# Optimization experiments

Hardware: AMD Instinct MI355X
Metric: run time of the kernel (lower is better)

The kernel has to match this reference:

```python
import jax, jax.numpy as jnp
import numpy as np

N_NODES = 131072       # 64 graphs * 2048 nodes
N_EDGES = 2097152      # avg degree 16
N_GRAPHS = 64
NODES_PER_GRAPH = 2048
D_IN = 128
D_EMB = 64
D_HID = 128
N_ACT = 2048


def setup_inputs() -> dict:
    key = jax.random.key(0)
    ks = jax.random.split(key, 12)
    s = lambda d: 1.0 / np.sqrt(d)
    return {
        "x": jax.random.normal(ks[0], (N_NODES, D_IN), dtype=jnp.float32),
        "edge_index": jax.random.randint(ks[1], (2, N_EDGES), 0, N_NODES, dtype=jnp.int32),
        "W1l": jax.random.normal(ks[2], (D_EMB, D_IN), dtype=jnp.float32) * s(D_IN),
        "b1l": jnp.zeros((D_EMB,), dtype=jnp.float32),
        "W1r": jax.random.normal(ks[3], (D_EMB, D_IN), dtype=jnp.float32) * s(D_IN),
        "W2l": jax.random.normal(ks[4], (D_EMB, D_EMB), dtype=jnp.float32) * s(D_EMB),
        "b2l": jnp.zeros((D_EMB,), dtype=jnp.float32),
        "W2r": jax.random.normal(ks[5], (D_EMB, D_EMB), dtype=jnp.float32) * s(D_EMB),
        "fc1_W": jax.random.normal(ks[6], (D_HID, D_EMB), dtype=jnp.float32) * s(D_EMB),
        "fc1_b": jnp.zeros((D_HID,), dtype=jnp.float32),
        "fc2_W": jax.random.normal(ks[7], (N_ACT, D_HID), dtype=jnp.float32) * s(D_HID),
        "fc2_b": jnp.zeros((N_ACT,), dtype=jnp.float32),
    }


def _sage_conv(x, src, dst, Wl, bl, Wr):
    # PyG SAGEConv (mean aggr): out = lin_l(mean_{j in N(i)} x_j) + lin_r(x_i)
    msg = x[src]                                              # [E, D] gather
    agg = jax.ops.segment_sum(msg, dst, num_segments=N_NODES)  # [N, D]
    cnt = jax.ops.segment_sum(jnp.ones((src.shape[0],), x.dtype), dst,
                              num_segments=N_NODES)
    mean = agg / jnp.maximum(cnt, 1.0)[:, None]
    return mean @ Wl.T + bl + x @ Wr.T


def reference(x, edge_index, W1l, b1l, W1r, W2l, b2l, W2r,
              fc1_W, fc1_b, fc2_W, fc2_b):
    src, dst = edge_index[0], edge_index[1]
    h1 = _sage_conv(x, src, dst, W1l, b1l, W1r)    # [N, D_EMB]
    h2 = _sage_conv(h1, src, dst, W2l, b2l, W2r)   # [N, D_EMB]
    g = h2.reshape(N_GRAPHS, NODES_PER_GRAPH, D_EMB).mean(axis=1)  # [B, D_EMB]
    h = jax.nn.relu(g @ fc1_W.T + fc1_b)
    q_values = h @ fc2_W.T + fc2_b                 # [B, N_ACT]
    return q_values
```

## Files before the change

### kernel.cpp

```cpp
#include <hip/hip_runtime.h>
#include <hip/hip_bf16.h>

#define D_IN 128
#define D_EMB 64

typedef float f32x2 __attribute__((ext_vector_type(2)));
typedef float f32x4v __attribute__((ext_vector_type(4)));
typedef short bf16x8 __attribute__((ext_vector_type(8)));

static __device__ __forceinline__ unsigned short f2bf(float f) {
  __hip_bfloat16 h = __float2bfloat16(f);
  return *(unsigned short*)&h;
}

__global__ __launch_bounds__(256) void wprep_mfma_k(const float* __restrict__ W,
                                                    unsigned short* __restrict__ out,
                                                    int K) {
  int tid = blockIdx.x * 256 + threadIdx.x;
  int total = (K / 32) * 4 * 64;
  if (tid >= total) return;
  int lane = tid & 63;
  int ct = (tid >> 6) & 3;
  int s = tid >> 8;
  int row = ct * 16 + (lane & 15);
  int kk = s * 32 + (lane >> 4) * 8;
  unsigned short tmp[8];
#pragma unroll
  for (int j = 0; j < 8; j++) tmp[j] = f2bf(W[row * K + kk + j]);
  *(uint4*)&out[(size_t)tid * 8] = *(uint4*)tmp;
}


__global__ __launch_bounds__(256) void bhist1_k(const int* __restrict__ dst,
                                                int* __restrict__ bh, int E) {
  __shared__ int h[256];
  const int t = threadIdx.x;
  h[t] = 0;
  __syncthreads();
  const int base = blockIdx.x * 2048;
#pragma unroll
  for (int j = 0; j < 8; j++) {
    int e = base + j * 256 + t;
    if (e < E) atomicAdd(&h[dst[e] >> 9], 1);
  }
  __syncthreads();
  bh[t * 1024 + blockIdx.x] = h[t];
}

__global__ __launch_bounds__(256) void scanA_k(int* __restrict__ bh,
                                               int* __restrict__ bintot) {
  __shared__ int sa[256], sb[256];
  const int t = threadIdx.x;
  int* row = bh + (size_t)blockIdx.x * 1024;
  int v0 = row[t * 4], v1 = row[t * 4 + 1], v2 = row[t * 4 + 2], v3 = row[t * 4 + 3];
  int sum = v0 + v1 + v2 + v3;
  sa[t] = sum;
  __syncthreads();
  int* in = sa;
  int* out = sb;
  for (int st = 1; st < 256; st <<= 1) {
    out[t] = in[t] + (t >= st ? in[t - st] : 0);
    __syncthreads();
    int* tmp = in; in = out; out = tmp;
  }
  int excl = in[t] - sum;
  row[t * 4] = excl;
  row[t * 4 + 1] = excl + v0;
  row[t * 4 + 2] = excl + v0 + v1;
  row[t * 4 + 3] = excl + v0 + v1 + v2;
  if (t == 255) bintot[blockIdx.x] = in[255];
}

__global__ __launch_bounds__(256) void scanB_k(const int* __restrict__ bintot,
                                               int* __restrict__ sbase) {
  __shared__ int sa[256], sb[256];
  const int t = threadIdx.x;
  int v = bintot[t];
  sa[t] = v;
  __syncthreads();
  int* in = sa;
  int* out = sb;
  for (int st = 1; st < 256; st <<= 1) {
    out[t] = in[t] + (t >= st ? in[t - st] : 0);
    __syncthreads();
    int* tmp = in; in = out; out = tmp;
  }
  sbase[t] = in[t] - v;
  if (t == 255) sbase[256] = in[255];
}

__global__ __launch_bounds__(256) void bfill1_k(const int* __restrict__ src,
                                                const int* __restrict__ dst,
                                                const int* __restrict__ bh,
                                                const int* __restrict__ sbase,
                                                unsigned int* __restrict__ bkt,
                                                int E) {
  __shared__ int hA[256], hB[256], runCur[256], gb[256];
  __shared__ int dcache[2048];
  __shared__ unsigned int sorted[2048];
  __shared__ unsigned short subb[2048];
  const int t = threadIdx.x;
  const int base = blockIdx.x * 2048;
  const int n = min(2048, E - base);
  hA[t] = 0;
  __syncthreads();
#pragma unroll
  for (int j = 0; j < 8; j++) {
    int idx = j * 256 + t;
    int e = base + idx;
    if (idx < n) {
      int d = dst[e];
      dcache[idx] = d;
      atomicAdd(&hA[d >> 9], 1);
    }
  }
  __syncthreads();
  int cnt = hA[t];
  int* in = hA;
  int* out = hB;
  for (int st = 1; st < 256; st <<= 1) {
    out[t] = in[t] + (t >= st ? in[t - st] : 0);
    __syncthreads();
    int* tmp = in; in = out; out = tmp;
  }
  int rs = in[t] - cnt;
  __syncthreads();
  hB[t] = rs;
  runCur[t] = rs;
  gb[t] = sbase[t] + bh[t * 1024 + blockIdx.x];
  __syncthreads();
#pragma unroll
  for (int j = 0; j < 8; j++) {
    int idx = j * 256 + t;
    int e = base + idx;
    if (idx < n) {
      int d = dcache[idx];
      int b = d >> 9;
      int lpos = atomicAdd(&runCur[b], 1);
      sorted[lpos] = ((unsigned)(d & 511) << 17) | (unsigned)src[e];
      subb[lpos] = (unsigned short)b;
    }
  }
  __syncthreads();
  for (int idx = t; idx < n; idx += 256) {
    int b = subb[idx];
    bkt[gb[b] + idx - hB[b]] = sorted[idx];
  }
}

__global__ __launch_bounds__(256) void deg4_k(const unsigned int* __restrict__ bkt,
                                              const int* __restrict__ sbase,
                                              int* __restrict__ deg) {
  __shared__ int h[512];
  const int t = threadIdx.x;
  h[t] = 0;
  h[t + 256] = 0;
  __syncthreads();
  const int i = blockIdx.x;
  const int lo = sbase[i], hi = sbase[i + 1];
  for (int e = lo + t; e < hi; e += 256) atomicAdd(&h[bkt[e] >> 17], 1);
  __syncthreads();
  deg[i * 512 + t] = h[t];
  deg[i * 512 + t + 256] = h[t + 256];
}

__global__ __launch_bounds__(256) void blocksum_k(const int* __restrict__ deg,
                                                  int* __restrict__ bsum) {
  __shared__ int sm[256];
  int t = threadIdx.x;
  sm[t] = deg[blockIdx.x * 256 + t];
  __syncthreads();
  for (int s = 128; s > 0; s >>= 1) {
    if (t < s) sm[t] += sm[t + s];
    __syncthreads();
  }
  if (t == 0) bsum[blockIdx.x] = sm[0];
}

__global__ __launch_bounds__(256) void scanbsum_k(int* __restrict__ bsum) {
  __shared__ int a[512], b[512];
  int t = threadIdx.x;
  a[t] = bsum[t];
  a[t + 256] = bsum[t + 256];
  __syncthreads();
  int* in = a;
  int* out = b;
  for (int st = 1; st < 512; st <<= 1) {
    for (int i = t; i < 512; i += 256) out[i] = in[i] + (i >= st ? in[i - st] : 0);
    __syncthreads();
    int* tmp = in; in = out; out = tmp;
  }
  for (int i = t; i < 512; i += 256) bsum[i] = (i == 0) ? 0 : in[i - 1];
}

__global__ __launch_bounds__(256) void rowptr_k(const int* __restrict__ deg,
                                                const int* __restrict__ bsumEx,
                                                int* __restrict__ rowPtr,
                                                float* __restrict__ invdeg) {
  __shared__ int a[256], b[256];
  int t = threadIdx.x;
  int i = blockIdx.x * 256 + t;
  int d = deg[i];
  a[t] = d;
  __syncthreads();
  int* in = a;
  int* out = b;
  for (int st = 1; st < 256; st <<= 1) {
    out[t] = in[t] + (t >= st ? in[t - st] : 0);
    __syncthreads();
    int* tmp = in; in = out; out = tmp;
  }
  int incl = in[t] + bsumEx[blockIdx.x];
  rowPtr[i + 1] = incl;
  invdeg[i] = 1.0f / fmaxf((float)d, 1.0f);
  if (i == 0) rowPtr[0] = 0;
}

#define CSR_CAP 12032
__global__ __launch_bounds__(256) void scat4_k(const unsigned int* __restrict__ bkt,
                                               const int* __restrict__ sbase,
                                               const int* __restrict__ rowPtr,
                                               int* __restrict__ csr) {
  __shared__ int cur[512];
  __shared__ int cbuf[CSR_CAP];
  const int t = threadIdx.x;
  const int i = blockIdx.x;
  const int node0 = i * 512;
  const int base0 = rowPtr[node0];
  cur[t] = rowPtr[node0 + t] - base0;
  cur[t + 256] = rowPtr[node0 + t + 256] - base0;
  __syncthreads();
  const int lo = sbase[i], hi = sbase[i + 1];
  for (int e = lo + t; e < hi; e += 256) {
    unsigned v = bkt[e];
    int pos = atomicAdd(&cur[v >> 17], 1);
    int sval = (int)(v & 0x1FFFFu);
    if (pos < CSR_CAP) cbuf[pos] = sval;
    else csr[base0 + pos] = sval;
  }
  __syncthreads();
  const int cnt = rowPtr[node0 + 512] - base0;
  const int lim = cnt < CSR_CAP ? cnt : CSR_CAP;
  for (int idx = t; idx < lim; idx += 256) csr[base0 + idx] = cbuf[idx];
}

template <int K, int DUAL>
__global__ __launch_bounds__(256) void gemm_mfma_k(const float4* __restrict__ x4,
                                                   const unsigned short* __restrict__ wb1,
                                                   const unsigned short* __restrict__ wb2,
                                                   const float* __restrict__ bias2,
                                                   unsigned char* __restrict__ out1,
                                                   float* __restrict__ out2) {
  constexpr int K4 = K / 4;
  constexpr int LROW = K + 8;
  __shared__ unsigned short sxb[64 * LROW];
  const int t = threadIdx.x;
  const int nb = blockIdx.x * 64;
#pragma unroll
  for (int idx = t; idx < 64 * K4; idx += 256) {
    int node = idx / K4, k4 = idx - node * K4;
    float4 v = x4[(size_t)(nb + node) * K4 + k4];
    ushort4 h;
    h.x = f2bf(v.x); h.y = f2bf(v.y); h.z = f2bf(v.z); h.w = f2bf(v.w);
    *(ushort4*)&sxb[node * LROW + k4 * 4] = h;
  }
  __syncthreads();
  const int lane = t & 63;
  const int wv = t >> 6;
  const int col = lane & 15;
  const int quad = lane >> 4;
  f32x4v acc1[4], acc2[4];
#pragma unroll
  for (int ct = 0; ct < 4; ct++) {
    acc1[ct] = (f32x4v){0.f, 0.f, 0.f, 0.f};
    if (DUAL) {
      float bj = bias2[ct * 16 + col];
      acc2[ct] = (f32x4v){bj, bj, bj, bj};
    }
  }
#pragma unroll
  for (int s = 0; s < K / 32; s++) {
    bf16x8 a = *(const bf16x8*)&sxb[(wv * 16 + col) * LROW + s * 32 + quad * 8];
#pragma unroll
    for (int ct = 0; ct < 4; ct++) {
      bf16x8 b1 = *(const bf16x8*)&wb1[(size_t)((s * 4 + ct) * 64 + lane) * 8];
      acc1[ct] = __builtin_amdgcn_mfma_f32_16x16x32_bf16(a, b1, acc1[ct], 0, 0, 0);
      if (DUAL) {
        bf16x8 b2 = *(const bf16x8*)&wb2[(size_t)((s * 4 + ct) * 64 + lane) * 8];
        acc2[ct] = __builtin_amdgcn_mfma_f32_16x16x32_bf16(a, b2, acc2[ct], 0, 0, 0);
      }
    }
  }
#pragma unroll
  for (int ct = 0; ct < 4; ct++) {
#pragma unroll
    for (int reg = 0; reg < 4; reg++) {
      int node = nb + wv * 16 + quad * 4 + reg;
      unsigned pk = (unsigned)__builtin_amdgcn_cvt_pk_fp8_f32(acc1[ct][reg],
                                                              acc1[ct][reg], 0, false);
      out1[(size_t)node * 64 + ct * 16 + col] = (unsigned char)(pk & 0xff);
      if (DUAL) out2[(size_t)node * 64 + ct * 16 + col] = acc2[ct][reg];
    }
  }
}

template <int WRITE_H>
__global__ __launch_bounds__(256) void gather_k(const uint4* __restrict__ yb,
                                                const int* __restrict__ csr,
                                                const int* __restrict__ rowPtr,
                                                const float* __restrict__ invdeg,
                                                float4* __restrict__ hio,
                                                float* __restrict__ pm) {
  __shared__ float sg[4][4][16];
  const int t = threadIdx.x;
  const int lane = t & 63;
  const int wv = t >> 6;
  const int q = lane & 3;
  const int nl = lane >> 2;
  const int nb = blockIdx.x * 64;
  const int n = nb + wv * 16 + nl;
  const int rp0 = rowPtr[n], rp1 = rowPtr[n + 1];
  float acc[16];
#pragma unroll
  for (int k = 0; k < 16; k++) acc[k] = 0.f;
  for (int e = rp0; e < rp1; e++) {
    int s = csr[e];
    uint4 v = yb[(size_t)s * 4 + q];
    f32x2 p;
    p = __builtin_amdgcn_cvt_pk_f32_fp8(v.x, false); acc[0] += p.x;  acc[1] += p.y;
    p = __builtin_amdgcn_cvt_pk_f32_fp8(v.x, true);  acc[2] += p.x;  acc[3] += p.y;
    p = __builtin_amdgcn_cvt_pk_f32_fp8(v.y, false); acc[4] += p.x;  acc[5] += p.y;
    p = __builtin_amdgcn_cvt_pk_f32_fp8(v.y, true);  acc[6] += p.x;  acc[7] += p.y;
    p = __builtin_amdgcn_cvt_pk_f32_fp8(v.z, false); acc[8] += p.x;  acc[9] += p.y;
    p = __builtin_amdgcn_cvt_pk_f32_fp8(v.z, true);  acc[10] += p.x; acc[11] += p.y;
    p = __builtin_amdgcn_cvt_pk_f32_fp8(v.w, false); acc[12] += p.x; acc[13] += p.y;
    p = __builtin_amdgcn_cvt_pk_f32_fp8(v.w, true);  acc[14] += p.x; acc[15] += p.y;
  }
  const float sc = invdeg[n];
  float gacc[16];
  if (WRITE_H) {
#pragma unroll
    for (int u = 0; u < 4; u++) {
      float4 o = hio[(size_t)n * 16 + q * 4 + u];
      float4 h = make_float4(acc[4 * u + 0] * sc + o.x, acc[4 * u + 1] * sc + o.y,
                             acc[4 * u + 2] * sc + o.z, acc[4 * u + 3] * sc + o.w);
      hio[(size_t)n * 16 + q * 4 + u] = h;
      gacc[4 * u + 0] = h.x; gacc[4 * u + 1] = h.y;
      gacc[4 * u + 2] = h.z; gacc[4 * u + 3] = h.w;
    }
  } else {
#pragma unroll
    for (int k = 0; k < 16; k++) gacc[k] = acc[k] * sc;
  }
#pragma unroll
  for (int m = 4; m <= 32; m <<= 1)
#pragma unroll
    for (int k = 0; k < 16; k++) gacc[k] += __shfl_xor(gacc[k], m, 64);
  if (nl == 0) {
#pragma unroll
    for (int k = 0; k < 16; k++) sg[wv][q][k] = gacc[k];
  }
  __syncthreads();
  if (t < 64) {
    int qq = t >> 4, k = t & 15;
    float tot = sg[0][qq][k] + sg[1][qq][k] + sg[2][qq][k] + sg[3][qq][k];
    pm[((size_t)(blockIdx.x >> 5) * 32 + (blockIdx.x & 31)) * 64 + t] = tot;
  }
}

__global__ __launch_bounds__(256) void reduce_part_k(const float* __restrict__ pm,
                                                     float* __restrict__ gm) {
  int idx = blockIdx.x * 256 + threadIdx.x;
  int b = idx >> 6, j = idx & 63;
  float acc = 0.0f;
  for (int blk = 0; blk < 32; blk++) acc += pm[((size_t)b * 32 + blk) * 64 + j];
  gm[idx] = acc * (1.0f / 2048.0f);
}

__global__ __launch_bounds__(256) void combine_k(const float* __restrict__ gmean2,
                                                 const float* __restrict__ gmean1,
                                                 const float* __restrict__ b2l,
                                                 const float* __restrict__ W2r,
                                                 float* __restrict__ g) {
  int idx = blockIdx.x * 256 + threadIdx.x;
  int b = idx >> 6, j = idx & 63;
  const float4* m4 = (const float4*)(gmean1 + b * 64);
  const float4* w4 = (const float4*)(W2r + j * 64);
  float acc = gmean2[idx] + b2l[j];
#pragma unroll
  for (int k4 = 0; k4 < 16; k4++) {
    float4 mv = m4[k4], wv = w4[k4];
    acc += mv.x * wv.x + mv.y * wv.y + mv.z * wv.z + mv.w * wv.w;
  }
  g[idx] = acc;
}

__global__ __launch_bounds__(256) void mlp1_k(const float* __restrict__ g,
                                              const float* __restrict__ fc1_W,
                                              const float* __restrict__ fc1_b,
                                              float* __restrict__ h) {
  int idx = blockIdx.x * 256 + threadIdx.x;
  int b = idx >> 7, k = idx & 127;
  const float4* g4 = (const float4*)(g + b * 64);
  const float4* w4 = (const float4*)(fc1_W + k * 64);
  float acc = fc1_b[k];
#pragma unroll
  for (int j4 = 0; j4 < 16; j4++) {
    float4 gv = g4[j4], wv = w4[j4];
    acc += gv.x * wv.x + gv.y * wv.y + gv.z * wv.z + gv.w * wv.w;
  }
  h[idx] = fmaxf(acc, 0.0f);
}

__global__ __launch_bounds__(256) void mlp2_k(const float* __restrict__ h,
                                              const float* __restrict__ fc2_W,
                                              const float* __restrict__ fc2_b,
                                              float* __restrict__ out) {
  __shared__ float4 sh[32];
  int b = blockIdx.x >> 3;
  int a = (blockIdx.x & 7) * 256 + threadIdx.x;
  if (threadIdx.x < 32) sh[threadIdx.x] = ((const float4*)(h + b * 128))[threadIdx.x];
  __syncthreads();
  const float4* w4 = (const float4*)(fc2_W + (size_t)a * 128);
  float acc = fc2_b[a];
#pragma unroll
  for (int k4 = 0; k4 < 32; k4++) {
    float4 hv = sh[k4], wv = w4[k4];
    acc += hv.x * wv.x + hv.y * wv.y + hv.z * wv.z + hv.w * wv.w;
  }
  out[b * 2048 + a] = acc;
}

extern "C" void kernel_launch(void* const* d_in, const int* in_sizes, int n_in,
                              void* d_out, int out_size, void* d_ws, size_t ws_size,
                              hipStream_t stream) {
  const float* x     = (const float*)d_in[0];
  const int*   ei    = (const int*)d_in[1];
  const float* W1l   = (const float*)d_in[2];
  const float* b1l   = (const float*)d_in[3];
  const float* W1r   = (const float*)d_in[4];
  const float* W2l   = (const float*)d_in[5];
  const float* b2l   = (const float*)d_in[6];
  const float* W2r   = (const float*)d_in[7];
  const float* fc1_W = (const float*)d_in[8];
  const float* fc1_b = (const float*)d_in[9];
  const float* fc2_W = (const float*)d_in[10];
  const float* fc2_b = (const float*)d_in[11];
  float* out = (float*)d_out;

  const int N = in_sizes[0] / D_IN;
  const int E = in_sizes[1] / 2;
  const int* src = ei;
  const int* dst = ei + E;

  char* ws = (char*)d_ws;
  int*   deg    = (int*)ws;     ws += (size_t)N * 4;
  int*   rowPtr = (int*)ws;     ws += (size_t)(N + 256) * 4;
  int*   bsum   = (int*)ws;     ws += 512 * 4;
  float* invdeg = (float*)ws;   ws += (size_t)N * 4;
  float* gmean1 = (float*)ws;   ws += 4096 * 4;
  float* gmean2 = (float*)ws;   ws += 4096 * 4;
  float* g      = (float*)ws;   ws += 4096 * 4;
  float* hbuf   = (float*)ws;   ws += 8192 * 4;
  unsigned short* wb1l = (unsigned short*)ws;  ws += 8192 * 2;
  unsigned short* wb1r = (unsigned short*)ws;  ws += 8192 * 2;
  unsigned short* wb2l = (unsigned short*)ws;  ws += 4096 * 2;
  int*   bh     = (int*)ws;     ws += (size_t)256 * 1024 * 4;
  int*   bintot = (int*)ws;     ws += 256 * 4;
  int*   sbase  = (int*)ws;     ws += 260 * 4;
  float* p1     = (float*)ws;   ws += (size_t)64 * 32 * 64 * 4;
  float* p2     = (float*)ws;   ws += (size_t)64 * 32 * 64 * 4;
  unsigned int* bkt = (unsigned int*)ws;  ws += (size_t)E * 4;
  int*   csr    = (int*)ws;     ws += (size_t)E * 4;
  unsigned char* bufA = (unsigned char*)ws;  ws += (size_t)64 * N;
  float* bufB   = (float*)ws;   ws += (size_t)64 * N * 4;
  size_t used = (size_t)(ws - (char*)d_ws);

  hipMemsetAsync(d_ws, 0, used, stream);

  wprep_mfma_k<<<4, 256, 0, stream>>>(W1l, wb1l, 128);
  wprep_mfma_k<<<4, 256, 0, stream>>>(W1r, wb1r, 128);
  wprep_mfma_k<<<2, 256, 0, stream>>>(W2l, wb2l, 64);

  const int nch = (E + 2047) >> 11;
  bhist1_k<<<nch, 256, 0, stream>>>(dst, bh, E);
  scanA_k<<<256, 256, 0, stream>>>(bh, bintot);
  scanB_k<<<1, 256, 0, stream>>>(bintot, sbase);
  bfill1_k<<<nch, 256, 0, stream>>>(src, dst, bh, sbase, bkt, E);
  deg4_k<<<256, 256, 0, stream>>>(bkt, sbase, deg);
  blocksum_k<<<N / 256, 256, 0, stream>>>(deg, bsum);
  scanbsum_k<<<1, 256, 0, stream>>>(bsum);
  rowptr_k<<<N / 256, 256, 0, stream>>>(deg, bsum, rowPtr, invdeg);
  scat4_k<<<256, 256, 0, stream>>>(bkt, sbase, rowPtr, csr);

  gemm_mfma_k<128, 1><<<N / 64, 256, 0, stream>>>((const float4*)x, wb1l, wb1r,
                                                  b1l, bufA, bufB);
  gather_k<1><<<N / 64, 256, 0, stream>>>((const uint4*)bufA, csr, rowPtr, invdeg,
                                          (float4*)bufB, p1);
  reduce_part_k<<<16, 256, 0, stream>>>(p1, gmean1);

  gemm_mfma_k<64, 0><<<N / 64, 256, 0, stream>>>((const float4*)bufB, wb2l, nullptr,
                                                 nullptr, bufA, nullptr);
  gather_k<0><<<N / 64, 256, 0, stream>>>((const uint4*)bufA, csr, rowPtr, invdeg,
                                          nullptr, p2);
  reduce_part_k<<<16, 256, 0, stream>>>(p2, gmean2);

  combine_k<<<16, 256, 0, stream>>>(gmean2, gmean1, b2l, W2r, g);
  mlp1_k<<<32, 256, 0, stream>>>(g, fc1_W, fc1_b, hbuf);
  mlp2_k<<<512, 256, 0, stream>>>(hbuf, fc2_W, fc2_b, out);
}
```

Baseline: 355.6 us.

## Pre-sort edges by source bucket before destination bucketing for gather locality

Adds a first bucketing pass that partitions edges by source-node bucket (src>>9), writing sorted src/dst arrays into reused scratch buffers, then runs the existing destination bucketing on that pre-sorted edge list. Within each destination row of the CSR, neighbours should then appear roughly in source order, which is meant to improve cache locality of the gather kernels. It adds a full extra histogram/scan/scatter pass over all edges.

```diff
diff --git a/kernel.cpp b/kernel.cpp
--- a/kernel.cpp
+++ b/kernel.cpp
@@ -31,7 +31,7 @@
 }
 
 
-__global__ __launch_bounds__(256) void bhist1_k(const int* __restrict__ dst,
+__global__ __launch_bounds__(256) void bhist1_k(const int* __restrict__ key,
                                                 int* __restrict__ bh, int E) {
   __shared__ int h[256];
   const int t = threadIdx.x;
@@ -41,7 +41,7 @@
 #pragma unroll
   for (int j = 0; j < 8; j++) {
     int e = base + j * 256 + t;
-    if (e < E) atomicAdd(&h[dst[e] >> 9], 1);
+    if (e < E) atomicAdd(&h[key[e] >> 9], 1);
   }
   __syncthreads();
   bh[t * 1024 + blockIdx.x] = h[t];
@@ -72,7 +72,7 @@
 }
 
 __global__ __launch_bounds__(256) void scanB_k(const int* __restrict__ bintot,
-                                               int* __restrict__ sbase) {
+                                               int* __restrict__ base) {
   __shared__ int sa[256], sb[256];
   const int t = threadIdx.x;
   int v = bintot[t];
@@ -85,8 +85,72 @@
     __syncthreads();
     int* tmp = in; in = out; out = tmp;
   }
-  sbase[t] = in[t] - v;
-  if (t == 255) sbase[256] = in[255];
+  base[t] = in[t] - v;
+  if (t == 255) base[256] = in[255];
+}
+
+__global__ __launch_bounds__(256) void sfill_k(const int* __restrict__ src,
+                                               const int* __restrict__ dst,
+                                               const int* __restrict__ sh,
+                                               const int* __restrict__ ssub,
+                                               int* __restrict__ srcS,
+                                               int* __restrict__ dstS, int E) {
+  __shared__ int hA[256], hB[256], runCur[256], gb[256];
+  __shared__ int scache[2048];
+  __shared__ int dcache[2048];
+  __shared__ int sortS[2048];
+  __shared__ int sortD[2048];
+  __shared__ unsigned short subb[2048];
+  const int t = threadIdx.x;
+  const int base = blockIdx.x * 2048;
+  const int n = min(2048, E - base);
+  hA[t] = 0;
+  __syncthreads();
+#pragma unroll
+  for (int j = 0; j < 8; j++) {
+    int idx = j * 256 + t;
+    int e = base + idx;
+    if (idx < n) {
+      int s = src[e];
+      scache[idx] = s;
+      dcache[idx] = dst[e];
+      atomicAdd(&hA[s >> 9], 1);
+    }
+  }
+  __syncthreads();
+  int cnt = hA[t];
+  int* in = hA;
+  int* out = hB;
+  for (int st = 1; st < 256; st <<= 1) {
+    out[t] = in[t] + (t >= st ? in[t - st] : 0);
+    __syncthreads();
+    int* tmp = in; in = out; out = tmp;
+  }
+  int rs = in[t] - cnt;
+  __syncthreads();
+  hB[t] = rs;
+  runCur[t] = rs;
+  gb[t] = ssub[t] + sh[t * 1024 + blockIdx.x];
+  __syncthreads();
+#pragma unroll
+  for (int j = 0; j < 8; j++) {
+    int idx = j * 256 + t;
+    if (idx < n) {
+      int s = scache[idx];
+      int b = s >> 9;
+      int lpos = atomicAdd(&runCur[b], 1);
+      sortS[lpos] = s;
+      sortD[lpos] = dcache[idx];
+      subb[lpos] = (unsigned short)b;
+    }
+  }
+  __syncthreads();
+  for (int idx = t; idx < n; idx += 256) {
+    int b = subb[idx];
+    int g = gb[b] + idx - hB[b];
+    srcS[g] = sortS[idx];
+    dstS[g] = sortD[idx];
+  }
 }
 
 __global__ __launch_bounds__(256) void bfill1_k(const int* __restrict__ src,
@@ -465,8 +529,10 @@
   unsigned short* wb1l = (unsigned short*)ws;  ws += 8192 * 2;
   unsigned short* wb1r = (unsigned short*)ws;  ws += 8192 * 2;
   unsigned short* wb2l = (unsigned short*)ws;  ws += 4096 * 2;
+  int*   sh     = (int*)ws;     ws += (size_t)256 * 1024 * 4;
   int*   bh     = (int*)ws;     ws += (size_t)256 * 1024 * 4;
-  int*   bintot = (int*)ws;     ws += 256 * 4;
+  int*   tot    = (int*)ws;     ws += 256 * 4;
+  int*   ssub   = (int*)ws;     ws += 260 * 4;
   int*   sbase  = (int*)ws;     ws += 260 * 4;
   float* p1     = (float*)ws;   ws += (size_t)64 * 32 * 64 * 4;
   float* p2     = (float*)ws;   ws += (size_t)64 * 32 * 64 * 4;
@@ -476,6 +542,9 @@
   float* bufB   = (float*)ws;   ws += (size_t)64 * N * 4;
   size_t used = (size_t)(ws - (char*)d_ws);
 
+  int* srcS = csr;
+  int* dstS = (int*)bufA;
+
   hipMemsetAsync(d_ws, 0, used, stream);
 
   wprep_mfma_k<<<4, 256, 0, stream>>>(W1l, wb1l, 128);
@@ -483,10 +552,14 @@
   wprep_mfma_k<<<2, 256, 0, stream>>>(W2l, wb2l, 64);
 
   const int nch = (E + 2047) >> 11;
-  bhist1_k<<<nch, 256, 0, stream>>>(dst, bh, E);
-  scanA_k<<<256, 256, 0, stream>>>(bh, bintot);
-  scanB_k<<<1, 256, 0, stream>>>(bintot, sbase);
-  bfill1_k<<<nch, 256, 0, stream>>>(src, dst, bh, sbase, bkt, E);
+  bhist1_k<<<nch, 256, 0, stream>>>(src, sh, E);
+  scanA_k<<<256, 256, 0, stream>>>(sh, tot);
+  scanB_k<<<1, 256, 0, stream>>>(tot, ssub);
+  sfill_k<<<nch, 256, 0, stream>>>(src, dst, sh, ssub, srcS, dstS, E);
+  bhist1_k<<<nch, 256, 0, stream>>>(dstS, bh, E);
+  scanA_k<<<256, 256, 0, stream>>>(bh, tot);
+  scanB_k<<<1, 256, 0, stream>>>(tot, sbase);
+  bfill1_k<<<nch, 256, 0, stream>>>(srcS, dstS, bh, sbase, bkt, E);
   deg4_k<<<256, 256, 0, stream>>>(bkt, sbase, deg);
   blocksum_k<<<N / 256, 256, 0, stream>>>(deg, bsum);
   scanbsum_k<<<1, 256, 0, stream>>>(bsum);
```

Measured after the change: 355.2 us. Within noise of the previous version (-0.1%).
